# Performance work log

Measured on AMD Instinct MI355X. Metric: run time of the kernel, lower is better.

## Reference

```python
import jax, jax.numpy as jnp
import numpy as np

B, L, D = 1, 4096, 1024
H, DH = 16, 64
BASE = 10000.0


def _rope_tables(L, dh, dtype=jnp.float32):
    inv_freq = 1.0 / (BASE ** (jnp.arange(0, dh, 2, dtype=jnp.float32) / dh))
    freqs = jnp.outer(jnp.arange(L, dtype=jnp.float32), inv_freq)  # [L, dh/2]
    return jnp.cos(freqs).astype(dtype), jnp.sin(freqs).astype(dtype)


def _apply_rope(x, cos, sin):
    # x: [B,H,L,dh]; cos/sin: [L,dh/2]
    x1, x2 = x[..., ::2], x[..., 1::2]
    c = cos[None, None]
    s = sin[None, None]
    return jnp.concatenate([x1 * c - x2 * s, x1 * s + x2 * c], axis=-1)


def setup_inputs() -> dict:
    key = jax.random.key(0)
    ks = jax.random.split(key, 5)
    x = jax.random.normal(ks[0], (B, L, D), dtype=jnp.float32)
    mask = jnp.tril(jnp.ones((L, L), dtype=jnp.int32))  # causal 0/1 mask
    sd = 1.0 / np.sqrt(D)
    Wq = jax.random.normal(ks[1], (D, D), dtype=jnp.float32) * sd
    Wk = jax.random.normal(ks[2], (D, D), dtype=jnp.float32) * sd
    Wv = jax.random.normal(ks[3], (D, D), dtype=jnp.float32) * sd
    Wo = jax.random.normal(ks[4], (D, D), dtype=jnp.float32) * sd
    return {"x": x, "mask": mask, "Wq": Wq, "Wk": Wk, "Wv": Wv, "Wo": Wo}


def reference(x, mask, Wq, Wk, Wv, Wo):
    b, l, d = x.shape
    scale = DH ** -0.5
    cos, sin = _rope_tables(l, DH, x.dtype)

    def heads(w):
        return (x @ w.T).reshape(b, l, H, DH).transpose(0, 2, 1, 3)  # [B,H,L,dh]

    q = _apply_rope(heads(Wq), cos, sin)
    k = _apply_rope(heads(Wk), cos, sin)
    v = heads(Wv)

    attn = jnp.einsum('bhqd,bhkd->bhqk', q, k) * scale
    attn = jnp.where(mask[:l, :l] == 0, -jnp.inf, attn)
    attn = jax.nn.softmax(attn, axis=-1)
    out = jnp.einsum('bhqk,bhkd->bhqd', attn, v)
    out = out.transpose(0, 2, 1, 3).reshape(b, l, d)
    return out @ Wo.T
```

## Files before the change

### kernel.cpp

```cpp
#include <hip/hip_runtime.h>
#include <math.h>

#define LSEQ   4096
#define DMODEL 1024
#define NH     16
#define DHEAD  64
#define PSTRIDE 40
#define MASKV  -30000.0f
#define C2SCALE 0.18033688f

typedef __attribute__((ext_vector_type(8))) short  bf16x8;
typedef __attribute__((ext_vector_type(4))) float  floatx4;
typedef unsigned short ushort_t;

#if __has_builtin(__builtin_amdgcn_exp2f)
#define EXP2F __builtin_amdgcn_exp2f
#else
#define EXP2F exp2f
#endif

__device__ __forceinline__ ushort_t f2bf(float x) {
  unsigned u = __builtin_bit_cast(unsigned, x);
  return (ushort_t)((u + 0x7fff + ((u >> 16) & 1)) >> 16);
}
__device__ __forceinline__ unsigned bf16pair(float a, float b) {
  return (unsigned)f2bf(a) | ((unsigned)f2bf(b) << 16);
}
__device__ __forceinline__ unsigned bfpack_trunc(float a, float b) {
  return __builtin_amdgcn_perm(__builtin_bit_cast(unsigned, b),
                               __builtin_bit_cast(unsigned, a), 0x07060302u);
}
__device__ __forceinline__ void gl_lds16(const ushort_t* g, ushort_t* l) {
  __builtin_amdgcn_global_load_lds(
      (const __attribute__((address_space(1))) void*)g,
      (__attribute__((address_space(3))) void*)l, 16, 0, 0);
}

__global__ void prep_fused(const float* __restrict__ x,  const float* __restrict__ wq,
                           const float* __restrict__ wk, const float* __restrict__ wv,
                           const float* __restrict__ wo, ushort_t* __restrict__ dst,
                           float2* __restrict__ rope) {
  if (blockIdx.x >= 8192) {
    const int idx = (blockIdx.x - 8192) * 256 + threadIdx.x;
    const int s = idx >> 5, t = idx & 31;
    const double invf = exp((double)t * -0.28782313662425572);
    const double ang = (double)s * invf;
    rope[idx] = make_float2((float)cos(ang), (float)sin(ang));
    return;
  }
  const size_t e = ((size_t)blockIdx.x * 256 + threadIdx.x) * 4;
  const float* src; size_t off;
  if      (e < (size_t)(4u << 20)) { src = x;  off = e; }
  else if (e < (size_t)(5u << 20)) { src = wq; off = e - (size_t)(4u << 20); }
  else if (e < (size_t)(6u << 20)) { src = wk; off = e - (size_t)(5u << 20); }
  else if (e < (size_t)(7u << 20)) { src = wv; off = e - (size_t)(6u << 20); }
  else                             { src = wo; off = e - (size_t)(7u << 20); }
  const float4 v = *(const float4*)(src + off);
  uint2 p; p.x = bf16pair(v.x, v.y); p.y = bf16pair(v.z, v.w);
  *(uint2*)(dst + e) = p;
}

__global__ __launch_bounds__(512, 2)
void gemm256_qkv(const ushort_t* __restrict__ A, const ushort_t* __restrict__ B,
                 const float2* __restrict__ rope,
                 ushort_t* __restrict__ Qo, ushort_t* __restrict__ Ko,
                 ushort_t* __restrict__ Vo) {
  __shared__ __align__(16) ushort_t smem[65536];
  const int tid  = threadIdx.x;
  const int w    = tid >> 6, lane = tid & 63;
  const int wr   = w >> 2,   wc   = w & 3;
  const int quad = lane >> 4, col = lane & 15;
  const int csw  = col & 7;
  const int bid = blockIdx.y * 12 + blockIdx.x;
  const int nb  = (bid & 7) * 24 + (bid >> 3);
  const int i0 = (nb % 12) * 256;
  const int j0 = (nb / 12) * 256;

  const ushort_t* Ab = A + (size_t)i0 * DMODEL;
  const ushort_t* Bb = B + (size_t)j0 * DMODEL;

  const int sr8 = lane >> 3;
  const int sc  = ((lane & 7) ^ sr8) * 8;

  floatx4 acc[8][4];
#pragma unroll
  for (int m = 0; m < 8; ++m)
#pragma unroll
    for (int n = 0; n < 4; ++n) acc[m][n] = (floatx4){0.f, 0.f, 0.f, 0.f};

  auto stageA = [&](int kt, int h) {
    ushort_t* dst = smem + (kt & 1) * 16384 + (h * 128 + w * 8) * 64;
    const ushort_t* src = Ab + (size_t)(h * 128 + w * 8 + sr8) * DMODEL + kt * 64 + sc;
    gl_lds16(src, dst);
    gl_lds16(src + (size_t)64 * DMODEL, dst + 4096);
  };
  auto stageB = [&](int kt, int h) {
    ushort_t* dst = smem + 32768 + (kt & 1) * 16384 + (h * 128 + w * 8) * 64;
    const ushort_t* src = Bb + (size_t)(h * 128 + w * 8 + sr8) * DMODEL + kt * 64 + sc;
    gl_lds16(src, dst);
    gl_lds16(src + (size_t)64 * DMODEL, dst + 4096);
  };

  stageA(0, 0); stageB(0, 0); stageA(0, 1); stageB(0, 1);
  asm volatile("s_waitcnt vmcnt(0)" ::: "memory");
  __builtin_amdgcn_s_barrier();

#pragma unroll 2
  for (int t = 0; t < 16; ++t) {
    const ushort_t* As_ = smem + (t & 1) * 16384;
    const ushort_t* Bs_ = smem + 32768 + (t & 1) * 16384;
    const bool pre = (t + 1 < 16);

    bf16x8 af[4], bfr[4];
#pragma unroll
    for (int n = 0; n < 4; ++n)
      bfr[n] = *(const bf16x8*)(Bs_ + (wc * 64 + n * 16 + col) * 64 + ((quad ^ csw) * 8));
#pragma unroll
    for (int m = 0; m < 4; ++m)
      af[m] = *(const bf16x8*)(As_ + (wr * 128 + m * 16 + col) * 64 + ((quad ^ csw) * 8));
    if (pre) { stageA(t + 1, 0); stageB(t + 1, 0); }
    __builtin_amdgcn_s_setprio(1);
#pragma unroll
    for (int m = 0; m < 4; ++m)
#pragma unroll
      for (int n = 0; n < 4; ++n)
        acc[m][n] = __builtin_amdgcn_mfma_f32_16x16x32_bf16(af[m], bfr[n], acc[m][n], 0, 0, 0);
    __builtin_amdgcn_s_setprio(0);
    __builtin_amdgcn_s_barrier();

#pragma unroll
    for (int m = 0; m < 4; ++m)
      af[m] = *(const bf16x8*)(As_ + (wr * 128 + (m + 4) * 16 + col) * 64 + ((quad ^ csw) * 8));
    if (pre) { stageA(t + 1, 1); stageB(t + 1, 1); }
    __builtin_amdgcn_s_setprio(1);
#pragma unroll
    for (int m = 0; m < 4; ++m)
#pragma unroll
      for (int n = 0; n < 4; ++n)
        acc[m + 4][n] = __builtin_amdgcn_mfma_f32_16x16x32_bf16(af[m], bfr[n], acc[m + 4][n], 0, 0, 0);
    __builtin_amdgcn_s_setprio(0);
    __builtin_amdgcn_s_barrier();

#pragma unroll
    for (int n = 0; n < 4; ++n)
      bfr[n] = *(const bf16x8*)(Bs_ + (wc * 64 + n * 16 + col) * 64 + (((4 + quad) ^ csw) * 8));
#pragma unroll
    for (int m = 0; m < 4; ++m)
      af[m] = *(const bf16x8*)(As_ + (wr * 128 + m * 16 + col) * 64 + (((4 + quad) ^ csw) * 8));
    __builtin_amdgcn_s_setprio(1);
#pragma unroll
    for (int m = 0; m < 4; ++m)
#pragma unroll
      for (int n = 0; n < 4; ++n)
        acc[m][n] = __builtin_amdgcn_mfma_f32_16x16x32_bf16(af[m], bfr[n], acc[m][n], 0, 0, 0);
    __builtin_amdgcn_s_setprio(0);
    __builtin_amdgcn_s_barrier();

#pragma unroll
    for (int m = 0; m < 4; ++m)
      af[m] = *(const bf16x8*)(As_ + (wr * 128 + (m + 4) * 16 + col) * 64 + (((4 + quad) ^ csw) * 8));
    __builtin_amdgcn_s_setprio(1);
#pragma unroll
    for (int m = 0; m < 4; ++m)
#pragma unroll
      for (int n = 0; n < 4; ++n)
        acc[m + 4][n] = __builtin_amdgcn_mfma_f32_16x16x32_bf16(af[m], bfr[n], acc[m + 4][n], 0, 0, 0);
    __builtin_amdgcn_s_setprio(0);
    asm volatile("s_waitcnt vmcnt(0)" ::: "memory");
    __builtin_amdgcn_s_barrier();
  }

  const int which = i0 >> 10;
#pragma unroll
  for (int m = 0; m < 8; ++m) {
    const int f0 = i0 + wr * 128 + m * 16 + quad * 4;
    const int h  = (f0 >> 6) & 15;
    const int d  = f0 & 63;
    if (which == 2) {
#pragma unroll
      for (int n = 0; n < 4; ++n) {
        const int s = j0 + wc * 64 + n * 16 + col;
#pragma unroll
        for (int r = 0; r < 4; ++r)
          Vo[(size_t)(h * DHEAD + d + r) * LSEQ + s] = f2bf(acc[m][n][r]);
      }
    } else {
      ushort_t* dst = which ? Ko : Qo;
      const float qs = which ? 1.0f : C2SCALE;
      const int t0 = d >> 1;
#pragma unroll
      for (int n = 0; n < 4; ++n) {
        const int s = j0 + wc * 64 + n * 16 + col;
        const float4 cst = *(const float4*)((const float*)rope + ((size_t)s << 6) + t0 * 2);
        ushort_t* ob = dst + ((size_t)h * LSEQ + s) * DHEAD;
        const float x1 = acc[m][n][0], x2 = acc[m][n][1];
        const float y1 = acc[m][n][2], y2 = acc[m][n][3];
        *(unsigned*)(ob + t0)      = bf16pair((x1 * cst.x - x2 * cst.y) * qs,
                                              (y1 * cst.z - y2 * cst.w) * qs);
        *(unsigned*)(ob + t0 + 32) = bf16pair((x1 * cst.y + x2 * cst.x) * qs,
                                              (y1 * cst.w + y2 * cst.z) * qs);
      }
    }
  }
}

template<int MODE>
__global__ __launch_bounds__(256)
void mfma_gemm(const ushort_t* __restrict__ A, const ushort_t* __restrict__ B,
               float* __restrict__ C, const float2* __restrict__ rope,
               ushort_t* __restrict__ Qo, ushort_t* __restrict__ Ko,
               ushort_t* __restrict__ Vo) {
  __shared__ ushort_t As[128 * 64];
  __shared__ ushort_t Bs[128 * 64];
  const int tid  = threadIdx.x;
  const int w    = tid >> 6, lane = tid & 63;
  const int wm   = w >> 1,   wn   = w & 1;
  const int quad = lane >> 4, col = lane & 15;
  const int csw  = col & 7;
  const int bid = blockIdx.y * 32 + blockIdx.x;
  const int nb  = (bid & 7) * 32 + (bid >> 3);
  const int i0 = (nb % 32) * 128;
  const int j0 = (nb / 32) * 128;

  const ushort_t* Ab = A + (size_t)i0 * DMODEL;
  const ushort_t* Bb = B + (size_t)j0 * DMODEL;

  floatx4 acc[4][4];
#pragma unroll
  for (int mt = 0; mt < 4; ++mt)
#pragma unroll
    for (int nt = 0; nt < 4; ++nt) acc[mt][nt] = (floatx4){0.f, 0.f, 0.f, 0.f};

  const int lrow = lane >> 3;
  const int lcol = ((lane & 7) ^ lrow) * 8;

  for (int k0 = 0; k0 < DMODEL; k0 += 64) {
    __syncthreads();
#pragma unroll
    for (int it = 0; it < 4; ++it) {
      const int rb = (it * 4 + w) * 8;
      gl_lds16(Ab + (size_t)(rb + lrow) * DMODEL + k0 + lcol, As + rb * 64);
      gl_lds16(Bb + (size_t)(rb + lrow) * DMODEL + k0 + lcol, Bs + rb * 64);
    }
    __syncthreads();

#pragma unroll
    for (int kk = 0; kk < 64; kk += 32) {
      const int cblk = (kk >> 3) + quad;
      bf16x8 af[4], bfr[4];
#pragma unroll
      for (int mt = 0; mt < 4; ++mt)
        af[mt] = *(const bf16x8*)(As + (wm * 64 + mt * 16 + col) * 64 +
                                  ((cblk ^ csw) * 8));
#pragma unroll
      for (int nt = 0; nt < 4; ++nt)
        bfr[nt] = *(const bf16x8*)(Bs + (wn * 64 + nt * 16 + col) * 64 +
                                   ((cblk ^ csw) * 8));
#pragma unroll
      for (int mt = 0; mt < 4; ++mt)
#pragma unroll
        for (int nt = 0; nt < 4; ++nt)
          acc[mt][nt] = __builtin_amdgcn_mfma_f32_16x16x32_bf16(
              af[mt], bfr[nt], acc[mt][nt], 0, 0, 0);
    }
  }

  if (MODE == 0) {
#pragma unroll
    for (int mt = 0; mt < 4; ++mt) {
      const int i = i0 + wm * 64 + mt * 16 + quad * 4;
#pragma unroll
      for (int nt = 0; nt < 4; ++nt) {
        const int j = j0 + wn * 64 + nt * 16 + col;
#pragma unroll
        for (int r = 0; r < 4; ++r)
          C[(size_t)(i + r) * DMODEL + j] = acc[mt][nt][r];
      }
    }
  } else {
    const int which = i0 >> 10;
#pragma unroll
    for (int mt = 0; mt < 4; ++mt) {
      const int f0 = i0 + wm * 64 + mt * 16 + quad * 4;
      const int h  = (f0 >> 6) & 15;
      const int d  = f0 & 63;
      if (which == 2) {
#pragma unroll
        for (int nt = 0; nt < 4; ++nt) {
          const int s = j0 + wn * 64 + nt * 16 + col;
#pragma unroll
          for (int r = 0; r < 4; ++r)
            Vo[(size_t)(h * DHEAD + d + r) * LSEQ + s] = f2bf(acc[mt][nt][r]);
        }
      } else {
        ushort_t* dst = which ? Ko : Qo;
        const float qs = which ? 1.0f : C2SCALE;
        const int t0 = d >> 1;
#pragma unroll
        for (int nt = 0; nt < 4; ++nt) {
          const int s = j0 + wn * 64 + nt * 16 + col;
          const float4 cst = *(const float4*)((const float*)rope + ((size_t)s << 6) + t0 * 2);
          ushort_t* ob = dst + ((size_t)h * LSEQ + s) * DHEAD;
          const float x1 = acc[mt][nt][0], x2 = acc[mt][nt][1];
          const float y1 = acc[mt][nt][2], y2 = acc[mt][nt][3];
          *(unsigned*)(ob + t0)      = bf16pair((x1 * cst.x - x2 * cst.y) * qs,
                                                (y1 * cst.z - y2 * cst.w) * qs);
          *(unsigned*)(ob + t0 + 32) = bf16pair((x1 * cst.y + x2 * cst.x) * qs,
                                                (y1 * cst.w + y2 * cst.z) * qs);
        }
      }
    }
  }
}

__global__ __launch_bounds__(1024, 4)
void attn_mfma(const ushort_t* __restrict__ Qh, const ushort_t* __restrict__ Kh,
               const ushort_t* __restrict__ Vt, ushort_t* __restrict__ Om) {
  const int h   = blockIdx.x;
  const int g   = blockIdx.y;
  const int tid = threadIdx.x;
  const int w     = tid >> 6;
  const int wl    = w & 3;
  const int half  = (w >> 2) & 1;
  const int ktpar = w >> 3;
  const int wg    = w & 7;
  const int lane = tid & 63;
  const int quad = lane >> 4;
  const int col  = lane & 15;
  const int csw  = col & 7;

  __shared__ __align__(16) char smem[139264];
  ushort_t* Ks   = (ushort_t*)smem;
  ushort_t* Vs   = (ushort_t*)(smem + 49152);
  ushort_t* Ps   = (ushort_t*)(smem + 98304);
  float*    Obuf = (float*)smem;
  __shared__ float lbuf[3][4][2][16];
  ushort_t* psw = Ps + w * (32 * PSTRIDE);

  const int srow = wg * 8 + (lane >> 3);
  const int scol = (((lane & 7) ^ ((lane >> 3) & 7)) * 8);

  for (int pass = 0; pass < 2; ++pass) {
    const int qb      = pass ? (31 - g) : g;
    const int qbase   = qb * 128 + wl * 32;
    const int nkt_max = 2 * qb + 2;
    const int nt2     = nkt_max >> 1;

    bf16x8 qf[2][2];
#pragma unroll
    for (int nq = 0; nq < 2; ++nq)
#pragma unroll
      for (int c = 0; c < 2; ++c)
        qf[nq][c] = *(const bf16x8*)(Qh +
            ((size_t)(h * LSEQ + qbase + nq * 16 + col)) * DHEAD + quad * 8 + c * 32);

    floatx4 ot[4][2];
#pragma unroll
    for (int md = 0; md < 4; ++md)
#pragma unroll
      for (int nq = 0; nq < 2; ++nq) ot[md][nq] = (floatx4){0.f, 0.f, 0.f, 0.f};
    float l_[2] = {0.f, 0.f};

    auto stage = [&](int kt, int b) {
      const int key0 = kt * 64;
      const int boff = (ktpar * 3 + b) * 4096;
      gl_lds16(Kh + ((size_t)(h * LSEQ + key0 + srow)) * DHEAD + scol,
               Ks + boff + wg * 512);
      gl_lds16(Vt + ((size_t)(h * DHEAD + srow)) * LSEQ + key0 + scol,
               Vs + boff + wg * 512);
    };

    stage(ktpar, 0);
    if (nt2 > 1) {
      stage(ktpar + 2, 1);
      asm volatile("s_waitcnt vmcnt(2)" ::: "memory");
    } else {
      asm volatile("s_waitcnt vmcnt(0)" ::: "memory");
    }
    __builtin_amdgcn_s_barrier();
    asm volatile("" ::: "memory");

    int bufn = 0;
    for (int ktt = 0; ktt < nt2; ++ktt) {
      const int kt  = 2 * ktt + ktpar;
      const bool pre = (ktt + 2 < nt2);
      if (pre) {
        const int nb = (bufn >= 1) ? bufn - 1 : 2;
        stage(kt + 4, nb);
      }

      const ushort_t* kb = Ks + (ktpar * 3 + bufn) * 4096;
      const ushort_t* vb = Vs + (ktpar * 3 + bufn) * 4096;

      bf16x8 kf[2][2];
#pragma unroll
      for (int mk = 0; mk < 2; ++mk)
#pragma unroll
        for (int c = 0; c < 2; ++c)
          kf[mk][c] = *(const bf16x8*)(kb + (half * 32 + mk * 16 + col) * 64 +
                                       (((c * 4 + quad) ^ csw) * 8));

      floatx4 st[2][2];
#pragma unroll
      for (int mk = 0; mk < 2; ++mk)
#pragma unroll
        for (int nq = 0; nq < 2; ++nq) st[mk][nq] = (floatx4){0.f, 0.f, 0.f, 0.f};
#pragma unroll
      for (int mk = 0; mk < 2; ++mk)
#pragma unroll
        for (int c = 0; c < 2; ++c)
#pragma unroll
          for (int nq = 0; nq < 2; ++nq)
            st[mk][nq] = __builtin_amdgcn_mfma_f32_16x16x32_bf16(
                kf[mk][c], qf[nq][c], st[mk][nq], 0, 0, 0);

      if (kt >= nkt_max - 2) {
        const int key0 = kt * 64 + half * 32;
#pragma unroll
        for (int mk = 0; mk < 2; ++mk) {
          const int keyb = key0 + mk * 16 + quad * 4;
#pragma unroll
          for (int nq = 0; nq < 2; ++nq) {
            const int q = qbase + nq * 16 + col;
#pragma unroll
            for (int r = 0; r < 4; ++r)
              if (keyb + r > q) st[mk][nq][r] = MASKV;
          }
        }
      }

#pragma unroll
      for (int mk = 0; mk < 2; ++mk)
#pragma unroll
        for (int nq = 0; nq < 2; ++nq) {
#pragma unroll
          for (int r = 0; r < 4; ++r) st[mk][nq][r] = EXP2F(st[mk][nq][r]);
          l_[nq] += (st[mk][nq][0] + st[mk][nq][1]) + (st[mk][nq][2] + st[mk][nq][3]);
        }

#pragma unroll
      for (int mk = 0; mk < 2; ++mk)
#pragma unroll
        for (int nq = 0; nq < 2; ++nq) {
          uint2 pk;
          pk.x = bfpack_trunc(st[mk][nq][0], st[mk][nq][1]);
          pk.y = bfpack_trunc(st[mk][nq][2], st[mk][nq][3]);
          *(uint2*)(psw + (nq * 16 + col) * PSTRIDE + mk * 16 + quad * 4) = pk;
        }
      bf16x8 pf[2];
#pragma unroll
      for (int nq = 0; nq < 2; ++nq)
        pf[nq] = *(const bf16x8*)(psw + (nq * 16 + col) * PSTRIDE + quad * 8);

      bf16x8 vf[4];
#pragma unroll
      for (int md = 0; md < 4; ++md)
        vf[md] = *(const bf16x8*)(vb + (md * 16 + col) * 64 +
                                  (((half * 4 + quad) ^ csw) * 8));
#pragma unroll
      for (int md = 0; md < 4; ++md)
#pragma unroll
        for (int nq = 0; nq < 2; ++nq)
          ot[md][nq] = __builtin_amdgcn_mfma_f32_16x16x32_bf16(
              vf[md], pf[nq], ot[md][nq], 0, 0, 0);

      if (pre) asm volatile("s_waitcnt vmcnt(2)" ::: "memory");
      else     asm volatile("s_waitcnt vmcnt(0)" ::: "memory");
      __builtin_amdgcn_s_barrier();
      asm volatile("" ::: "memory");
      bufn = (bufn == 2) ? 0 : bufn + 1;
    }

    float lr[2];
#pragma unroll
    for (int nq = 0; nq < 2; ++nq) {
      float ls = l_[nq];
      ls += __shfl_xor(ls, 16);
      ls += __shfl_xor(ls, 32);
      lr[nq] = ls;
    }

    const int di = ((half << 1) | ktpar) - 1;
    if (di >= 0) {
#pragma unroll
      for (int nq = 0; nq < 2; ++nq) {
        if (quad == 0) lbuf[di][wl][nq][col] = lr[nq];
#pragma unroll
        for (int md = 0; md < 4; ++md)
          *(float4*)(Obuf + di * 8704 + ((wl * 2 + nq) * 16 + col) * 68 + md * 16 + quad * 4) =
              (float4){ot[md][nq][0], ot[md][nq][1], ot[md][nq][2], ot[md][nq][3]};
      }
    }
    __syncthreads();

    if (di < 0) {
#pragma unroll
      for (int nq = 0; nq < 2; ++nq) {
        const float inv = 1.0f / (lr[nq] + lbuf[0][wl][nq][col] +
                                  lbuf[1][wl][nq][col] + lbuf[2][wl][nq][col]);
        const int q = qbase + nq * 16 + col;
#pragma unroll
        for (int md = 0; md < 4; ++md) {
          const int ob_off = ((wl * 2 + nq) * 16 + col) * 68 + md * 16 + quad * 4;
          const float4 o0 = *(const float4*)(Obuf + ob_off);
          const float4 o1 = *(const float4*)(Obuf + 8704 + ob_off);
          const float4 o2 = *(const float4*)(Obuf + 17408 + ob_off);
          uint2 pk;
          pk.x = bf16pair((ot[md][nq][0] + o0.x + o1.x + o2.x) * inv,
                          (ot[md][nq][1] + o0.y + o1.y + o2.y) * inv);
          pk.y = bf16pair((ot[md][nq][2] + o0.z + o1.z + o2.z) * inv,
                          (ot[md][nq][3] + o0.w + o1.w + o2.w) * inv);
          *(uint2*)(Om + (size_t)q * DMODEL + h * DHEAD + md * 16 + quad * 4) = pk;
        }
      }
    }
    __syncthreads();
  }
}

extern "C" void kernel_launch(void* const* d_in, const int* in_sizes, int n_in,
                              void* d_out, int out_size, void* d_ws, size_t ws_size,
                              hipStream_t stream) {
  const float* x  = (const float*)d_in[0];
  const float* Wq = (const float*)d_in[2];
  const float* Wk = (const float*)d_in[3];
  const float* Wv = (const float*)d_in[4];
  const float* Wo = (const float*)d_in[5];
  float* out = (float*)d_out;

  const size_t M1 = (size_t)1 << 20;
  ushort_t* xb  = (ushort_t*)d_ws;
  ushort_t* Wb  = xb  + 4 * M1;
  ushort_t* wob = Wb  + 3 * M1;
  ushort_t* Qh  = wob + 1 * M1;
  ushort_t* Kh  = Qh  + 4 * M1;
  ushort_t* Vt  = Kh  + 4 * M1;
  ushort_t* Om  = Vt  + 4 * M1;
  float2*   rope = (float2*)(Om + 4 * M1);

  prep_fused<<<8704, 256, 0, stream>>>(x, Wq, Wk, Wv, Wo, xb, rope);
  gemm256_qkv<<<dim3(12, 16), 512, 0, stream>>>(
      Wb, xb, rope, Qh, Kh, Vt);
  attn_mfma<<<dim3(NH, 16), 1024, 0, stream>>>(Qh, Kh, Vt, Om);
  mfma_gemm<0><<<dim3(32, 8), 256, 0, stream>>>(
      Om, wob, out, nullptr, nullptr, nullptr, nullptr);
}
```

Before: 241.1 us.

## Retile QKV GEMM to 192x256 tiles with triple-buffered A staging

The QKV projection GEMM now uses 192-row A tiles instead of 256, so the grid grows from 192 to 256 blocks and fills the GPU's compute units more evenly. A is triple-buffered in LDS and prefetched two k-steps ahead, with partial vmcnt waits to overlap loads with MFMA work. B stays double-buffered. Because a tile can now straddle the Q/K/V boundary, the epilogue picks Q/K/V per row. LDS use grows slightly and per-block arithmetic intensity drops.

Measured after the change: 235.2 us. 2.4% less time.

```diff
diff --git a/kernel.cpp b/kernel.cpp
--- a/kernel.cpp
+++ b/kernel.cpp
@@ -65,16 +65,16 @@
                  const float2* __restrict__ rope,
                  ushort_t* __restrict__ Qo, ushort_t* __restrict__ Ko,
                  ushort_t* __restrict__ Vo) {
-  __shared__ __align__(16) ushort_t smem[65536];
+  __shared__ __align__(16) ushort_t smem[69632];
   const int tid  = threadIdx.x;
   const int w    = tid >> 6, lane = tid & 63;
   const int wr   = w >> 2,   wc   = w & 3;
   const int quad = lane >> 4, col = lane & 15;
   const int csw  = col & 7;
-  const int bid = blockIdx.y * 12 + blockIdx.x;
-  const int nb  = (bid & 7) * 24 + (bid >> 3);
-  const int i0 = (nb % 12) * 256;
-  const int j0 = (nb / 12) * 256;
+  const int bid = blockIdx.x;
+  const int nb  = (bid & 7) * 32 + (bid >> 3);
+  const int i0 = (nb & 15) * 192;
+  const int j0 = (nb >> 4) * 256;
 
   const ushort_t* Ab = A + (size_t)i0 * DMODEL;
   const ushort_t* Bb = B + (size_t)j0 * DMODEL;
@@ -82,46 +82,44 @@
   const int sr8 = lane >> 3;
   const int sc  = ((lane & 7) ^ sr8) * 8;
 
-  floatx4 acc[8][4];
-#pragma unroll
-  for (int m = 0; m < 8; ++m)
+  floatx4 acc[6][4];
+#pragma unroll
+  for (int m = 0; m < 6; ++m)
 #pragma unroll
     for (int n = 0; n < 4; ++n) acc[m][n] = (floatx4){0.f, 0.f, 0.f, 0.f};
 
   auto stageA = [&](int kt, int h) {
-    ushort_t* dst = smem + (kt & 1) * 16384 + (h * 128 + w * 8) * 64;
-    const ushort_t* src = Ab + (size_t)(h * 128 + w * 8 + sr8) * DMODEL + kt * 64 + sc;
-    gl_lds16(src, dst);
-    gl_lds16(src + (size_t)64 * DMODEL, dst + 4096);
+    ushort_t* dst = smem + (kt % 3) * 12288 + (h * 64 + w * 8) * 64;
+    gl_lds16(Ab + (size_t)(h * 64 + w * 8 + sr8) * DMODEL + kt * 64 + sc, dst);
   };
   auto stageB = [&](int kt, int h) {
-    ushort_t* dst = smem + 32768 + (kt & 1) * 16384 + (h * 128 + w * 8) * 64;
-    const ushort_t* src = Bb + (size_t)(h * 128 + w * 8 + sr8) * DMODEL + kt * 64 + sc;
-    gl_lds16(src, dst);
-    gl_lds16(src + (size_t)64 * DMODEL, dst + 4096);
+    ushort_t* dst = smem + 36864 + (kt & 1) * 16384 + (h * 64 + w * 8) * 64;
+    gl_lds16(Bb + (size_t)(h * 64 + w * 8 + sr8) * DMODEL + kt * 64 + sc, dst);
   };
 
-  stageA(0, 0); stageB(0, 0); stageA(0, 1); stageB(0, 1);
-  asm volatile("s_waitcnt vmcnt(0)" ::: "memory");
+  stageA(0, 0); stageA(0, 1); stageA(0, 2);
+  stageB(0, 0); stageB(0, 1); stageB(0, 2); stageB(0, 3);
+  stageA(1, 0); stageA(1, 1); stageA(1, 2);
+  asm volatile("s_waitcnt vmcnt(3)" ::: "memory");
   __builtin_amdgcn_s_barrier();
 
-#pragma unroll 2
   for (int t = 0; t < 16; ++t) {
-    const ushort_t* As_ = smem + (t & 1) * 16384;
-    const ushort_t* Bs_ = smem + 32768 + (t & 1) * 16384;
-    const bool pre = (t + 1 < 16);
-
-    bf16x8 af[4], bfr[4];
+    const ushort_t* As_ = smem + (t % 3) * 12288;
+    const ushort_t* Bs_ = smem + 36864 + (t & 1) * 16384;
+    const bool preB = (t + 1 < 16);
+    const bool preA = (t + 2 < 16);
+
+    bf16x8 af[3], bfr[4];
 #pragma unroll
     for (int n = 0; n < 4; ++n)
       bfr[n] = *(const bf16x8*)(Bs_ + (wc * 64 + n * 16 + col) * 64 + ((quad ^ csw) * 8));
 #pragma unroll
-    for (int m = 0; m < 4; ++m)
-      af[m] = *(const bf16x8*)(As_ + (wr * 128 + m * 16 + col) * 64 + ((quad ^ csw) * 8));
-    if (pre) { stageA(t + 1, 0); stageB(t + 1, 0); }
+    for (int m = 0; m < 3; ++m)
+      af[m] = *(const bf16x8*)(As_ + (wr * 96 + m * 16 + col) * 64 + ((quad ^ csw) * 8));
+    if (preB) { stageB(t + 1, 0); stageB(t + 1, 1); }
     __builtin_amdgcn_s_setprio(1);
 #pragma unroll
-    for (int m = 0; m < 4; ++m)
+    for (int m = 0; m < 3; ++m)
 #pragma unroll
       for (int n = 0; n < 4; ++n)
         acc[m][n] = __builtin_amdgcn_mfma_f32_16x16x32_bf16(af[m], bfr[n], acc[m][n], 0, 0, 0);
@@ -129,15 +127,15 @@
     __builtin_amdgcn_s_barrier();
 
 #pragma unroll
-    for (int m = 0; m < 4; ++m)
-      af[m] = *(const bf16x8*)(As_ + (wr * 128 + (m + 4) * 16 + col) * 64 + ((quad ^ csw) * 8));
-    if (pre) { stageA(t + 1, 1); stageB(t + 1, 1); }
+    for (int m = 0; m < 3; ++m)
+      af[m] = *(const bf16x8*)(As_ + (wr * 96 + (m + 3) * 16 + col) * 64 + ((quad ^ csw) * 8));
+    if (preB) { stageB(t + 1, 2); stageB(t + 1, 3); }
     __builtin_amdgcn_s_setprio(1);
 #pragma unroll
-    for (int m = 0; m < 4; ++m)
+    for (int m = 0; m < 3; ++m)
 #pragma unroll
       for (int n = 0; n < 4; ++n)
-        acc[m + 4][n] = __builtin_amdgcn_mfma_f32_16x16x32_bf16(af[m], bfr[n], acc[m + 4][n], 0, 0, 0);
+        acc[m + 3][n] = __builtin_amdgcn_mfma_f32_16x16x32_bf16(af[m], bfr[n], acc[m + 3][n], 0, 0, 0);
     __builtin_amdgcn_s_setprio(0);
     __builtin_amdgcn_s_barrier();
 
@@ -145,11 +143,12 @@
     for (int n = 0; n < 4; ++n)
       bfr[n] = *(const bf16x8*)(Bs_ + (wc * 64 + n * 16 + col) * 64 + (((4 + quad) ^ csw) * 8));
 #pragma unroll
-    for (int m = 0; m < 4; ++m)
-      af[m] = *(const bf16x8*)(As_ + (wr * 128 + m * 16 + col) * 64 + (((4 + quad) ^ csw) * 8));
+    for (int m = 0; m < 3; ++m)
+      af[m] = *(const bf16x8*)(As_ + (wr * 96 + m * 16 + col) * 64 + (((4 + quad) ^ csw) * 8));
+    if (preA) { stageA(t + 2, 0); stageA(t + 2, 1); stageA(t + 2, 2); }
     __builtin_amdgcn_s_setprio(1);
 #pragma unroll
-    for (int m = 0; m < 4; ++m)
+    for (int m = 0; m < 3; ++m)
 #pragma unroll
       for (int n = 0; n < 4; ++n)
         acc[m][n] = __builtin_amdgcn_mfma_f32_16x16x32_bf16(af[m], bfr[n], acc[m][n], 0, 0, 0);
@@ -157,25 +156,26 @@
     __builtin_amdgcn_s_barrier();
 
 #pragma unroll
-    for (int m = 0; m < 4; ++m)
-      af[m] = *(const bf16x8*)(As_ + (wr * 128 + (m + 4) * 16 + col) * 64 + (((4 + quad) ^ csw) * 8));
+    for (int m = 0; m < 3; ++m)
+      af[m] = *(const bf16x8*)(As_ + (wr * 96 + (m + 3) * 16 + col) * 64 + (((4 + quad) ^ csw) * 8));
     __builtin_amdgcn_s_setprio(1);
 #pragma unroll
-    for (int m = 0; m < 4; ++m)
+    for (int m = 0; m < 3; ++m)
 #pragma unroll
       for (int n = 0; n < 4; ++n)
-        acc[m + 4][n] = __builtin_amdgcn_mfma_f32_16x16x32_bf16(af[m], bfr[n], acc[m + 4][n], 0, 0, 0);
+        acc[m + 3][n] = __builtin_amdgcn_mfma_f32_16x16x32_bf16(af[m], bfr[n], acc[m + 3][n], 0, 0, 0);
     __builtin_amdgcn_s_setprio(0);
-    asm volatile("s_waitcnt vmcnt(0)" ::: "memory");
+    if (preA) asm volatile("s_waitcnt vmcnt(3)" ::: "memory");
+    else      asm volatile("s_waitcnt vmcnt(0)" ::: "memory");
     __builtin_amdgcn_s_barrier();
   }
 
-  const int which = i0 >> 10;
-#pragma unroll
-  for (int m = 0; m < 8; ++m) {
-    const int f0 = i0 + wr * 128 + m * 16 + quad * 4;
-    const int h  = (f0 >> 6) & 15;
-    const int d  = f0 & 63;
+#pragma unroll
+  for (int m = 0; m < 6; ++m) {
+    const int f0    = i0 + wr * 96 + m * 16 + quad * 4;
+    const int which = f0 >> 10;
+    const int h     = (f0 >> 6) & 15;
+    const int d     = f0 & 63;
     if (which == 2) {
 #pragma unroll
       for (int n = 0; n < 4; ++n) {
@@ -539,8 +539,7 @@
   float2*   rope = (float2*)(Om + 4 * M1);
 
   prep_fused<<<8704, 256, 0, stream>>>(x, Wq, Wk, Wv, Wo, xb, rope);
-  gemm256_qkv<<<dim3(12, 16), 512, 0, stream>>>(
-      Wb, xb, rope, Qh, Kh, Vt);
+  gemm256_qkv<<<256, 512, 0, stream>>>(Wb, xb, rope, Qh, Kh, Vt);
   attn_mfma<<<dim3(NH, 16), 1024, 0, stream>>>(Qh, Kh, Vt, Om);
   mfma_gemm<0><<<dim3(32, 8), 256, 0, stream>>>(
       Om, wob, out, nullptr, nullptr, nullptr, nullptr);
```
